# Kernel tuning notes

Measured on AMD Instinct MI355X. Metric: run time of the kernel, lower is better.

The kernel has to match this reference:

```python
import jax, jax.numpy as jnp
import numpy as np
from jax import lax

# Dims
HID = 2048          # hidden_size
DI = 4096           # d_inner = expand * hidden
NH = 64             # mamba heads
P = 64              # head dim
N = 128             # d_state
G = 1               # n_groups
K = 4               # conv kernel
IM = 8192           # MLP intermediate
BB, L = 2, 2048
EPS = 1e-5
CONV_DIM = DI + 2 * G * N            # 4352
D_IN_PROJ = 2 * DI + 2 * G * N + NH  # 8512


def rmsnorm(x, w, eps=EPS):
    v = jnp.mean(jnp.square(x), axis=-1, keepdims=True)
    return x * jax.lax.rsqrt(v + eps) * w


def setup_inputs() -> dict:
    key = jax.random.key(0)
    ks = jax.random.split(key, 16)
    s = 0.02
    return {
        "positions": jnp.broadcast_to(jnp.arange(L, dtype=jnp.int32), (BB, L)),
        "hidden_states": jax.random.normal(ks[0], (BB, L, HID), jnp.float32),
        "residual": jax.random.normal(ks[1], (BB, L, HID), jnp.float32),
        "in_proj_w": jax.random.normal(ks[2], (D_IN_PROJ, HID), jnp.float32) * s,
        "conv_w": jax.random.normal(ks[3], (CONV_DIM, K), jnp.float32) * 0.2,
        "conv_b": jax.random.normal(ks[4], (CONV_DIM,), jnp.float32) * 0.02,
        "A_log": jnp.log(jnp.arange(1, NH + 1, dtype=jnp.float32)),
        "D": jnp.ones((NH,), jnp.float32),
        "dt_bias": jax.random.uniform(ks[5], (NH,), jnp.float32, -4.0, -2.0),
        "mixer_norm_w": jnp.ones((DI,), jnp.float32),
        "out_proj_w": jax.random.normal(ks[6], (HID, DI), jnp.float32) * s,
        "input_ln_w": jnp.ones((HID,), jnp.float32),
        "pre_ff_ln_w": jnp.ones((HID,), jnp.float32),
        "gate_up_w": jax.random.normal(ks[7], (2 * IM, HID), jnp.float32) * s,
        "down_w": jax.random.normal(ks[8], (HID, IM), jnp.float32) * s,
    }


def reference(positions, hidden_states, residual, in_proj_w, conv_w, conv_b,
              A_log, D, dt_bias, mixer_norm_w, out_proj_w, input_ln_w,
              pre_ff_ln_w, gate_up_w, down_w):
    del positions  # not used by the mamba mixer math
    B_, Lq, _ = hidden_states.shape

    # --- input RMSNorm with fused residual add ---
    residual = hidden_states + residual
    hs = rmsnorm(residual, input_ln_w)

    # --- Mamba2 mixer ---
    proj = jnp.einsum('bld,ed->ble', hs, in_proj_w)   # [B,L,D_IN_PROJ]
    z = proj[..., :DI]
    xBC = proj[..., DI:DI + CONV_DIM]
    dt = proj[..., DI + CONV_DIM:]                    # [B,L,NH]

    # causal depthwise conv (kernel K) + SiLU
    xp = jnp.pad(xBC, ((0, 0), (K - 1, 0), (0, 0)))
    conv = conv_b
    for k in range(K):
        conv = conv + xp[:, k:k + Lq, :] * conv_w[:, k]
    xBC = jax.nn.silu(conv)

    x = xBC[..., :DI].reshape(B_, Lq, NH, P)
    Bm = xBC[..., DI:DI + G * N].reshape(B_, Lq, G, N)
    Cm = xBC[..., DI + G * N:].reshape(B_, Lq, G, N)
    rep = NH // G
    Bm = jnp.repeat(Bm, rep, axis=2)                  # [B,L,NH,N]
    Cm = jnp.repeat(Cm, rep, axis=2)

    dt = jax.nn.softplus(dt + dt_bias)                # [B,L,NH]
    A = -jnp.exp(A_log)                               # [NH]
    dA = jnp.exp(dt * A)                              # [B,L,NH]

    def step(h, inp):
        x_t, B_t, C_t, dA_t, dt_t = inp               # [B,NH,P],[B,NH,N],[B,NH,N],[B,NH],[B,NH]
        h = dA_t[..., None, None] * h + \
            (dt_t[..., None, None] * x_t[..., None]) * B_t[:, :, None, :]
        y = jnp.einsum('bhpn,bhn->bhp', h, C_t)
        return h, y

    xs = (x.transpose(1, 0, 2, 3), Bm.transpose(1, 0, 2, 3),
          Cm.transpose(1, 0, 2, 3), dA.transpose(1, 0, 2), dt.transpose(1, 0, 2))
    h0 = jnp.zeros((B_, NH, P, N), hidden_states.dtype)
    _, ys = lax.scan(step, h0, xs)                    # [L,B,NH,P]
    y = ys.transpose(1, 0, 2, 3) + D[None, None, :, None] * x
    y = y.reshape(B_, Lq, DI)

    # gated RMSNorm (Mixer2RMSNormGated, n_groups=1)
    y = y * jax.nn.silu(z)
    y = rmsnorm(y, mixer_norm_w)
    mamba_out = jnp.einsum('bld,hd->blh', y, out_proj_w)

    # --- pre-FF RMSNorm with fused residual add ---
    residual2 = mamba_out + residual
    hs2 = rmsnorm(residual2, pre_ff_ln_w)

    # --- gated MLP (SiluAndMul) ---
    gu = jnp.einsum('bld,ed->ble', hs2, gate_up_w)    # [B,L,2*IM]
    act = jax.nn.silu(gu[..., :IM]) * gu[..., IM:]
    out = jnp.einsum('bli,hi->blh', act, down_w)
    return out, residual2
```

## Files before the change

### kernel.cpp

```cpp
#include <hip/hip_runtime.h>

#define T_TOK 4096
#define HID   2048
#define DI    4096
#define NH    64
#define PDIM  64
#define NSTATE 128
#define IM    8192
#define LSEQ  2048
#define CONVD 4352
#define DPROJ 8512
#define DPADR 8704
#define QC    64
#define NCH   32

typedef __bf16 bf16x8 __attribute__((ext_vector_type(8)));
typedef float  f32x4  __attribute__((ext_vector_type(4)));

__device__ __forceinline__ unsigned short f2bf(float f) {
  unsigned u = __float_as_uint(f);
  u = (u + 0x7fffu + ((u >> 16) & 1u)) >> 16;
  return (unsigned short)u;
}
__device__ __forceinline__ float bf2f(unsigned short h) {
  return __uint_as_float(((unsigned)h) << 16);
}
__device__ __forceinline__ float siluf(float x) {
  return x / (1.f + __expf(-x));
}

#define GLL(gaddr, laddr) __builtin_amdgcn_global_load_lds( \
    (const __attribute__((address_space(1))) void*)(gaddr), \
    (__attribute__((address_space(3))) void*)(laddr), 16, 0, 0)

__device__ __forceinline__ void cvt8(const float* __restrict__ s, unsigned short* __restrict__ d) {
  float4 v0 = *(const float4*)s;
  float4 v1 = *(const float4*)(s + 4);
  unsigned short o[8];
  o[0] = f2bf(v0.x); o[1] = f2bf(v0.y); o[2] = f2bf(v0.z); o[3] = f2bf(v0.w);
  o[4] = f2bf(v1.x); o[5] = f2bf(v1.y); o[6] = f2bf(v1.z); o[7] = f2bf(v1.w);
  *(uint4*)d = *(const uint4*)o;
}

#define CV_IN_END  2228224ULL
#define CV_OUT_END 3276800ULL
#define CV_GU_END  7471104ULL
#define CV_DN_END  9568256ULL

__global__ __launch_bounds__(256)
void k_cvt_all(const float* __restrict__ w_in, const float* __restrict__ w_out,
               const float* __restrict__ w_gu, const float* __restrict__ w_dn,
               unsigned short* __restrict__ d_in, unsigned short* __restrict__ d_out,
               unsigned short* __restrict__ d_gu, unsigned short* __restrict__ d_dn) {
  size_t gid = (size_t)blockIdx.x * 256 + threadIdx.x;
  if (gid < CV_IN_END) {
    size_t idx8 = gid * 8;
    int r = (int)(idx8 >> 11), k = (int)(idx8 & 2047);
    if (r < DPROJ) {
      cvt8(&w_in[(size_t)r * HID + k], d_in + idx8);
    } else {
      uint4 z = {0, 0, 0, 0};
      *(uint4*)(d_in + idx8) = z;
    }
  } else if (gid < CV_OUT_END) {
    size_t idx8 = (gid - CV_IN_END) * 8;
    cvt8(w_out + idx8, d_out + idx8);
  } else if (gid < CV_GU_END) {
    size_t idx8 = (gid - CV_OUT_END) * 8;
    int r = (int)(idx8 >> 11), k = (int)(idx8 & 2047);
    int g = r >> 6, j = r & 63;
    int srcr = (j < 32) ? (g * 32 + j) : (IM + g * 32 + (j - 32));
    cvt8(&w_gu[(size_t)srcr * HID + k], d_gu + idx8);
  } else if (gid < CV_DN_END) {
    size_t idx8 = (gid - CV_GU_END) * 8;
    cvt8(w_dn + idx8, d_dn + idx8);
  }
}

template <int EPI, int BM>
__global__ __launch_bounds__(512, 2)
void gemm8(const unsigned short* __restrict__ A, const unsigned short* __restrict__ W,
           int K, int ldo, void* __restrict__ outp,
           const float* __restrict__ resid) {
  constexpr int MREP  = BM / 32;
  constexpr int ABYT  = BM * 128;
  constexpr int BUFB  = ABYT + 32768;
  constexpr int NTM   = 4096 / BM;
  __shared__ __align__(16) char smem[2 * BUFB];
  const int t = threadIdx.x;
  const int w = t >> 6, l = t & 63;
  const int lr = l & 15, hi = l >> 4;
  const int wr = w >> 2, wc = w & 3;

  const int q = (int)gridDim.x >> 3;
  const int bid = blockIdx.x;
  const int id2 = (bid & 7) * q + (bid >> 3);
  const int tn = id2 / NTM, tm = id2 % NTM;
  const int m0b = tm * BM, n0b = tn << 8;

  const int srow = t >> 3;
  const int scole = ((t & 7) << 3) ^ ((t & 32) ? 16 : 0) ^ ((t & 64) ? 32 : 0);
  const unsigned short* Ag = A + (size_t)(m0b + srow) * K + scole;
  const unsigned short* Wg = W + (size_t)(n0b + srow) * K + scole;
  const int ldsw = w * 1024;

  const int fa = ((lr & 4) ? 32 : 0) | ((lr & 8) ? 64 : 0);
  const int arow = (wr * (BM / 2) + lr) * 128 + hi * 16;
  const int brow = (wc * 64 + lr) * 128 + hi * 16;
  const int aoff0 = arow ^ fa, aoff1 = (arow + 64) ^ fa;
  const int boff0 = brow ^ fa, boff1 = (brow + 64) ^ fa;

#define ISSUE_A(jt, bb) do {                                                    \
    _Pragma("unroll")                                                           \
    for (int p_ = 0; p_ < BM / 64; ++p_)                                        \
      GLL(Ag + (size_t)(p_ * 64) * K + (size_t)(jt) * 64,                       \
          smem + (bb) * BUFB + p_ * 8192 + ldsw); } while (0)
#define ISSUE_B(jt, bb) do {                                                    \
    _Pragma("unroll")                                                           \
    for (int p_ = 0; p_ < 4; ++p_)                                              \
      GLL(Wg + (size_t)(p_ * 64) * K + (size_t)(jt) * 64,                       \
          smem + (bb) * BUFB + ABYT + p_ * 8192 + ldsw); } while (0)

#define RDF(off, base) (*(const bf16x8*)((base) + (off)))
#define MF(P, x, y, c0, c1, c2, c3) do {                                                     \
    acc[2*(P)  ][0] = __builtin_amdgcn_mfma_f32_16x16x32_bf16((x),(c0),acc[2*(P)  ][0],0,0,0);\
    acc[2*(P)+1][0] = __builtin_amdgcn_mfma_f32_16x16x32_bf16((y),(c0),acc[2*(P)+1][0],0,0,0);\
    acc[2*(P)  ][1] = __builtin_amdgcn_mfma_f32_16x16x32_bf16((x),(c1),acc[2*(P)  ][1],0,0,0);\
    acc[2*(P)+1][1] = __builtin_amdgcn_mfma_f32_16x16x32_bf16((y),(c1),acc[2*(P)+1][1],0,0,0);\
    acc[2*(P)  ][2] = __builtin_amdgcn_mfma_f32_16x16x32_bf16((x),(c2),acc[2*(P)  ][2],0,0,0);\
    acc[2*(P)+1][2] = __builtin_amdgcn_mfma_f32_16x16x32_bf16((y),(c2),acc[2*(P)+1][2],0,0,0);\
    acc[2*(P)  ][3] = __builtin_amdgcn_mfma_f32_16x16x32_bf16((x),(c3),acc[2*(P)  ][3],0,0,0);\
    acc[2*(P)+1][3] = __builtin_amdgcn_mfma_f32_16x16x32_bf16((y),(c3),acc[2*(P)+1][3],0,0,0);\
    } while (0)

  f32x4 acc[MREP][4];
#pragma unroll
  for (int m = 0; m < MREP; m++)
#pragma unroll
    for (int n = 0; n < 4; n++) acc[m][n] = (f32x4){0.f, 0.f, 0.f, 0.f};

  const int nkt = K >> 6;
  ISSUE_A(0, 0); ISSUE_B(0, 0);

  for (int j = 0; j < nkt; ++j) {
    const int cur = j & 1;
    const char* Ab = smem + cur * BUFB;
    const char* Bb = Ab + ABYT;
    asm volatile("s_waitcnt vmcnt(0)" ::: "memory");
    __builtin_amdgcn_s_barrier();
    __builtin_amdgcn_sched_barrier(0);
    if (j + 1 < nkt) { ISSUE_A(j + 1, cur ^ 1); ISSUE_B(j + 1, cur ^ 1); }
    bf16x8 b0 = RDF(boff0, Bb), b1 = RDF(boff0 + 2048, Bb),
           b2 = RDF(boff0 + 4096, Bb), b3 = RDF(boff0 + 6144, Bb);
    bf16x8 af0 = RDF(aoff0, Ab), af1 = RDF(aoff0 + 2048, Ab);
    bf16x8 af2, af3, b4, b5, b6, b7;
    if constexpr (MREP == 8) {
      af2 = RDF(aoff0 + 4096, Ab); af3 = RDF(aoff0 + 6144, Ab);
      MF(0, af0, af1, b0, b1, b2, b3);
      af0 = RDF(aoff0 + 8192, Ab); af1 = RDF(aoff0 + 10240, Ab);
      MF(1, af2, af3, b0, b1, b2, b3);
      af2 = RDF(aoff0 + 12288, Ab); af3 = RDF(aoff0 + 14336, Ab);
      MF(2, af0, af1, b0, b1, b2, b3);
      b4 = RDF(boff1, Bb); b5 = RDF(boff1 + 2048, Bb);
      b6 = RDF(boff1 + 4096, Bb); b7 = RDF(boff1 + 6144, Bb);
      af0 = RDF(aoff1, Ab); af1 = RDF(aoff1 + 2048, Ab);
      MF(3, af2, af3, b0, b1, b2, b3);
      af2 = RDF(aoff1 + 4096, Ab); af3 = RDF(aoff1 + 6144, Ab);
      MF(0, af0, af1, b4, b5, b6, b7);
      af0 = RDF(aoff1 + 8192, Ab); af1 = RDF(aoff1 + 10240, Ab);
      MF(1, af2, af3, b4, b5, b6, b7);
      af2 = RDF(aoff1 + 12288, Ab); af3 = RDF(aoff1 + 14336, Ab);
      MF(2, af0, af1, b4, b5, b6, b7);
      MF(3, af2, af3, b4, b5, b6, b7);
    } else {
      af2 = RDF(aoff0 + 4096, Ab); af3 = RDF(aoff0 + 6144, Ab);
      MF(0, af0, af1, b0, b1, b2, b3);
      b4 = RDF(boff1, Bb); b5 = RDF(boff1 + 2048, Bb);
      b6 = RDF(boff1 + 4096, Bb); b7 = RDF(boff1 + 6144, Bb);
      af0 = RDF(aoff1, Ab); af1 = RDF(aoff1 + 2048, Ab);
      MF(1, af2, af3, b0, b1, b2, b3);
      af2 = RDF(aoff1 + 4096, Ab); af3 = RDF(aoff1 + 6144, Ab);
      MF(0, af0, af1, b4, b5, b6, b7);
      MF(1, af2, af3, b4, b5, b6, b7);
    }
  }

  if constexpr (EPI == 0) {
    unsigned short* op = (unsigned short*)outp;
#pragma unroll
    for (int m = 0; m < MREP; m++)
#pragma unroll
      for (int n = 0; n < 4; n++)
#pragma unroll
        for (int r = 0; r < 4; r++) {
          int row = m0b + wr * (BM / 2) + m * 16 + hi * 4 + r;
          int col = n0b + wc * 64 + n * 16 + lr;
          op[(size_t)row * ldo + col] = f2bf(acc[m][n][r]);
        }
  } else if constexpr (EPI == 2) {
    unsigned short* op = (unsigned short*)outp;
    const int gbase = (n0b + wc * 64) >> 1;
#pragma unroll
    for (int m = 0; m < MREP; m++)
#pragma unroll
      for (int n = 0; n < 2; n++)
#pragma unroll
        for (int r = 0; r < 4; r++) {
          int row = m0b + wr * (BM / 2) + m * 16 + hi * 4 + r;
          int col = gbase + n * 16 + lr;
          float g = acc[m][n][r], u = acc[m][n + 2][r];
          op[(size_t)row * ldo + col] = f2bf(siluf(g) * u);
        }
  } else {
    float* op = (float*)outp;
#pragma unroll
    for (int m = 0; m < MREP; m++)
#pragma unroll
      for (int n = 0; n < 4; n++)
#pragma unroll
        for (int r = 0; r < 4; r++) {
          int row = m0b + wr * (BM / 2) + m * 16 + hi * 4 + r;
          int col = n0b + wc * 64 + n * 16 + lr;
          float v = acc[m][n][r];
          if constexpr (EPI == 1) v += resid[(size_t)row * ldo + col];
          op[(size_t)row * ldo + col] = v;
        }
  }
#undef ISSUE_A
#undef ISSUE_B
#undef RDF
#undef MF
}

__device__ __forceinline__ float block_reduce_sum256(float v, float* sred) {
#pragma unroll
  for (int m = 32; m; m >>= 1) v += __shfl_xor(v, m);
  int t = threadIdx.x;
  if ((t & 63) == 0) sred[t >> 6] = v;
  __syncthreads();
  return sred[0] + sred[1] + sred[2] + sred[3];
}

__global__ __launch_bounds__(256)
void k_addnorm(const float* __restrict__ hin, const float* __restrict__ rin,
               const float* __restrict__ wln, float* __restrict__ rout,
               unsigned short* __restrict__ hbf) {
  __shared__ float sred[4];
  const int tok = blockIdx.x, t = threadIdx.x;
  const size_t base = (size_t)tok * HID + t * 8;
  float4 a0 = *(const float4*)&hin[base];
  float4 a1 = *(const float4*)&hin[base + 4];
  float4 b0 = *(const float4*)&rin[base];
  float4 b1 = *(const float4*)&rin[base + 4];
  float v[8] = {a0.x + b0.x, a0.y + b0.y, a0.z + b0.z, a0.w + b0.w,
                a1.x + b1.x, a1.y + b1.y, a1.z + b1.z, a1.w + b1.w};
  float ss = 0.f;
#pragma unroll
  for (int j = 0; j < 8; j++) ss += v[j] * v[j];
  float tot = block_reduce_sum256(ss, sred);
  float rms = rsqrtf(tot * (1.f / HID) + 1e-5f);
  *(float4*)&rout[base] = (float4){v[0], v[1], v[2], v[3]};
  *(float4*)&rout[base + 4] = (float4){v[4], v[5], v[6], v[7]};
  float4 w0 = *(const float4*)&wln[t * 8];
  float4 w1 = *(const float4*)&wln[t * 8 + 4];
  float wa[8] = {w0.x, w0.y, w0.z, w0.w, w1.x, w1.y, w1.z, w1.w};
  unsigned short o[8];
#pragma unroll
  for (int j = 0; j < 8; j++) o[j] = f2bf(v[j] * rms * wa[j]);
  *(ushort4*)&hbf[base] = *(ushort4*)&o[0];
  *(ushort4*)&hbf[base + 4] = *(ushort4*)&o[4];
}

__global__ __launch_bounds__(256)
void k_rmsnorm_bf(const float* __restrict__ src, const float* __restrict__ wln,
                  unsigned short* __restrict__ dst) {
  __shared__ float sred[4];
  const int tok = blockIdx.x, t = threadIdx.x;
  const size_t base = (size_t)tok * HID + t * 8;
  float4 a0 = *(const float4*)&src[base];
  float4 a1 = *(const float4*)&src[base + 4];
  float v[8] = {a0.x, a0.y, a0.z, a0.w, a1.x, a1.y, a1.z, a1.w};
  float ss = 0.f;
#pragma unroll
  for (int j = 0; j < 8; j++) ss += v[j] * v[j];
  float tot = block_reduce_sum256(ss, sred);
  float rms = rsqrtf(tot * (1.f / HID) + 1e-5f);
  float4 w0 = *(const float4*)&wln[t * 8];
  float4 w1 = *(const float4*)&wln[t * 8 + 4];
  float wa[8] = {w0.x, w0.y, w0.z, w0.w, w1.x, w1.y, w1.z, w1.w};
  unsigned short o[8];
#pragma unroll
  for (int j = 0; j < 8; j++) o[j] = f2bf(v[j] * rms * wa[j]);
  *(ushort4*)&dst[base] = *(ushort4*)&o[0];
  *(ushort4*)&dst[base + 4] = *(ushort4*)&o[4];
}

__global__ __launch_bounds__(256)
void k_gatenorm(const unsigned short* __restrict__ ybuf, const unsigned short* __restrict__ projbf,
                const float* __restrict__ wmix, unsigned short* __restrict__ ynorm) {
  __shared__ float sred[4];
  const int tok = blockIdx.x, t = threadIdx.x;
  const size_t yb = (size_t)tok * DI;
  const size_t pb = (size_t)tok * DPADR;
  float g[16];
  float ss = 0.f;
#pragma unroll
  for (int j = 0; j < 16; j++) {
    int idx = j * 256 + t;
    float yv = bf2f(ybuf[yb + idx]);
    float z = bf2f(projbf[pb + idx]);
    float gg = yv * siluf(z);
    g[j] = gg;
    ss += gg * gg;
  }
  float tot = block_reduce_sum256(ss, sred);
  float rms = rsqrtf(tot * (1.f / DI) + 1e-5f);
#pragma unroll
  for (int j = 0; j < 16; j++) {
    int idx = j * 256 + t;
    ynorm[yb + idx] = f2bf(g[j] * rms * wmix[idx]);
  }
}

__global__ __launch_bounds__(256)
void k_conv(const unsigned short* __restrict__ projbf, const float* __restrict__ cw,
            const float* __restrict__ cb, const float* __restrict__ dt_bias,
            unsigned short* __restrict__ xbf, unsigned short* __restrict__ bcbf,
            float* __restrict__ dtg) {
  const int c = blockIdx.x * 256 + threadIdx.x;
  const int tk = blockIdx.y;
  if (c < CONVD) {
    const int lpos = tk & (LSEQ - 1);
    float4 wv = *(const float4*)&cw[c * 4];
    float wk[4] = {wv.x, wv.y, wv.z, wv.w};
    float acc = cb[c];
#pragma unroll
    for (int k = 0; k < 4; k++) {
      int lp = lpos - 3 + k;
      if (lp >= 0) acc += bf2f(projbf[(size_t)(tk - 3 + k) * DPADR + DI + c]) * wk[k];
    }
    unsigned short r = f2bf(siluf(acc));
    if (c < DI) xbf[(size_t)tk * DI + c] = r;
    else        bcbf[(size_t)tk * 256 + (c - DI)] = r;
  } else if (c < CONVD + NH) {
    const int hh = c - CONVD;
    float x = bf2f(projbf[(size_t)tk * DPADR + DI + c]) + dt_bias[hh];
    float dt = (x > 20.f) ? x : log1pf(__expf(x));
    dtg[(size_t)tk * NH + hh] = dt;
  }
}

__global__ __launch_bounds__(256)
void k_ssd1(const unsigned short* __restrict__ xbf, const unsigned short* __restrict__ bcbf,
            const float* __restrict__ dtg, const float* __restrict__ A_log,
            const float* __restrict__ Dv, unsigned short* __restrict__ ybuf,
            unsigned short* __restrict__ Sc, float* __restrict__ dtsum) {
  __shared__ __align__(16) char smem[60928];
  unsigned short* sBs  = (unsigned short*)(smem);
  unsigned short* sCs  = (unsigned short*)(smem + 16384);
  unsigned short* sMs  = (unsigned short*)(smem + 16384);
  unsigned short* sBsT = (unsigned short*)(smem + 32768);
  unsigned short* sXsT = (unsigned short*)(smem + 51200);
  float* sdt = (float*)(smem + 60416);
  float* sdl = (float*)(smem + 60672);

  const int bi = blockIdx.x;
  const int ch = bi & 31, h = (bi >> 5) & 63, b = bi >> 11;
  const int bh = b * NH + h;
  const int tok0 = b * LSEQ + ch * QC;
  const int t = threadIdx.x;
  const int w = t >> 6, l = t & 63, lr = l & 15, hi = l >> 4;
  const float Ah = -__expf(A_log[h]);
  const float Dh = Dv[h];

  {
    const int srow = t >> 4, scol = (t & 15) * 8;
#pragma unroll
    for (int i = 0; i < 4; i++) {
      const unsigned short* gb = bcbf + (size_t)(tok0 + srow + 16 * i) * 256 + scol;
      GLL(gb, (char*)sBs + i * 4096 + w * 1024);
      GLL(gb + 128, (char*)sCs + i * 4096 + w * 1024);
    }
  }
  if (t < QC) sdt[t] = dtg[(size_t)(tok0 + t) * NH + h];
  __syncthreads();
  if (t < QC) sdl[t] = sdt[t];
  __syncthreads();
  for (int off = 1; off < QC; off <<= 1) {
    float v = 0.f;
    if (t < QC && t >= off) v = sdl[t - off];
    __syncthreads();
    if (t < QC) sdl[t] += v;
    __syncthreads();
  }

  {
    const int s = t >> 2;
    const float DlQ = sdl[QC - 1];
    const float csc = __expf(Ah * (DlQ - sdl[s])) * sdt[s];
    const int n0 = (t & 3) * 32;
#pragma unroll
    for (int j = 0; j < 32; j++) {
      float bv = bf2f(sBs[s * 128 + n0 + j]);
      sBsT[(n0 + j) * 72 + s] = f2bf(csc * bv);
    }
    const int p0 = (t & 3) * 16;
    const unsigned short* gx = xbf + (size_t)(tok0 + s) * DI + h * 64 + p0;
    union { uint4 v; unsigned short u[8]; } x0, x1;
    x0.v = *(const uint4*)gx;
    x1.v = *(const uint4*)(gx + 8);
#pragma unroll
    for (int j = 0; j < 8; j++) {
      sXsT[(p0 + j) * 72 + s] = x0.u[j];
      sXsT[(p0 + 8 + j) * 72 + s] = x1.u[j];
    }
  }
  __syncthreads();

  f32x4 accS[4];
#pragma unroll
  for (int jf = 0; jf < 4; jf++) accS[jf] = (f32x4){0.f, 0.f, 0.f, 0.f};
#pragma unroll
  for (int ks = 0; ks < 4; ks++) {
    bf16x8 a = *(const bf16x8*)&sBs[(w * 16 + lr) * 128 + ks * 32 + hi * 8];
#pragma unroll
    for (int jf = 0; jf < 4; jf++) {
      bf16x8 bbq = *(const bf16x8*)&sCs[(jf * 16 + lr) * 128 + ks * 32 + hi * 8];
      accS[jf] = __builtin_amdgcn_mfma_f32_16x16x32_bf16(a, bbq, accS[jf], 0, 0, 0);
    }
  }
  __syncthreads();

  {
    const int s0 = w * 16 + hi * 4;
#pragma unroll
    for (int jf = 0; jf < 4; jf++) {
      const int tt = jf * 16 + lr;
      const float dlt = sdl[tt];
      unsigned short mv[4];
#pragma unroll
      for (int r = 0; r < 4; r++) {
        const int ss = s0 + r;
        float val = 0.f;
        if (ss <= tt) val = accS[jf][r] * __expf(Ah * (dlt - sdl[ss])) * sdt[ss];
        mv[r] = f2bf(val);
      }
      *(ushort4*)&sMs[tt * 72 + s0] = *(ushort4*)mv;
    }
  }
  __syncthreads();

  {
    f32x4 accY[4];
#pragma unroll
    for (int jf = 0; jf < 4; jf++) accY[jf] = (f32x4){0.f, 0.f, 0.f, 0.f};
#pragma unroll
    for (int ks = 0; ks < 2; ks++) {
      bf16x8 a = *(const bf16x8*)&sMs[(w * 16 + lr) * 72 + ks * 32 + hi * 8];
#pragma unroll
      for (int jf = 0; jf < 4; jf++) {
        bf16x8 bbq = *(const bf16x8*)&sXsT[(jf * 16 + lr) * 72 + ks * 32 + hi * 8];
        accY[jf] = __builtin_amdgcn_mfma_f32_16x16x32_bf16(a, bbq, accY[jf], 0, 0, 0);
      }
    }
#pragma unroll
    for (int jf = 0; jf < 4; jf++)
#pragma unroll
      for (int r = 0; r < 4; r++) {
        const int tt = w * 16 + hi * 4 + r;
        const int pp = jf * 16 + lr;
        float xv = bf2f(sXsT[pp * 72 + tt]);
        ybuf[(size_t)(tok0 + tt) * DI + h * 64 + pp] = f2bf(accY[jf][r] + Dh * xv);
      }
  }

  {
    f32x4 accT[8];
#pragma unroll
    for (int jf = 0; jf < 8; jf++) accT[jf] = (f32x4){0.f, 0.f, 0.f, 0.f};
#pragma unroll
    for (int ks = 0; ks < 2; ks++) {
      bf16x8 a = *(const bf16x8*)&sXsT[(w * 16 + lr) * 72 + ks * 32 + hi * 8];
#pragma unroll
      for (int jf = 0; jf < 8; jf++) {
        bf16x8 bbq = *(const bf16x8*)&sBsT[(jf * 16 + lr) * 72 + ks * 32 + hi * 8];
        accT[jf] = __builtin_amdgcn_mfma_f32_16x16x32_bf16(a, bbq, accT[jf], 0, 0, 0);
      }
    }
    unsigned short* sc = Sc + ((size_t)bh * NCH + ch) * (PDIM * NSTATE);
#pragma unroll
    for (int jf = 0; jf < 8; jf++)
#pragma unroll
      for (int r = 0; r < 4; r++) {
        const int pp = w * 16 + hi * 4 + r;
        const int nn = jf * 16 + lr;
        sc[pp * NSTATE + nn] = f2bf(accT[jf][r]);
      }
  }
  if (t == 0) dtsum[bh * NCH + ch] = sdl[QC - 1];
}

__global__ __launch_bounds__(256)
void k_ssd2(const float* __restrict__ A_log, const float* __restrict__ dtsum,
            unsigned short* __restrict__ ScHt) {
  const int blk = blockIdx.x;
  const int bh = blk >> 3, pg = blk & 7;
  const int t = threadIdx.x;
  const int p = pg * 8 + (t >> 5), n0 = (t & 31) * 4;
  const int h = bh & 63;
  const float Ah = -__expf(A_log[h]);
  float H[4] = {0.f, 0.f, 0.f, 0.f};
  for (int c = 0; c < NCH; c++) {
    size_t base = (((size_t)bh * NCH + c) * PDIM + p) * NSTATE + n0;
    ushort4 sv = *(const ushort4*)&ScHt[base];
    float dec = __expf(Ah * dtsum[bh * NCH + c]);
    ushort4 hv;
    hv.x = f2bf(H[0]); hv.y = f2bf(H[1]); hv.z = f2bf(H[2]); hv.w = f2bf(H[3]);
    *(ushort4*)&ScHt[base] = hv;
    H[0] = dec * H[0] + bf2f(sv.x);
    H[1] = dec * H[1] + bf2f(sv.y);
    H[2] = dec * H[2] + bf2f(sv.z);
    H[3] = dec * H[3] + bf2f(sv.w);
  }
}

__global__ __launch_bounds__(256)
void k_ssd3(const unsigned short* __restrict__ bcbf, const unsigned short* __restrict__ Ht,
            const float* __restrict__ dtg, const float* __restrict__ A_log,
            unsigned short* __restrict__ ybuf) {
  __shared__ __align__(16) char smem[33280];
  unsigned short* sCs = (unsigned short*)(smem);
  unsigned short* sHt = (unsigned short*)(smem + 16384);
  float* sdt = (float*)(smem + 32768);
  float* sdl = (float*)(smem + 33024);

  const int bi = blockIdx.x;
  const int ch = bi & 31, h = (bi >> 5) & 63, b = bi >> 11;
  const int bh = b * NH + h;
  const int tok0 = b * LSEQ + ch * QC;
  const int t = threadIdx.x;
  const int w = t >> 6, l = t & 63, lr = l & 15, hi = l >> 4;
  const float Ah = -__expf(A_log[h]);

  {
    const int srow = t >> 4, scol = (t & 15) * 8;
    const unsigned short* gh = Ht + ((size_t)bh * NCH + ch) * (PDIM * NSTATE);
#pragma unroll
    for (int i = 0; i < 4; i++) {
      const unsigned short* gc = bcbf + (size_t)(tok0 + srow + 16 * i) * 256 + 128 + scol;
      GLL(gc, (char*)sCs + i * 4096 + w * 1024);
      GLL(gh + i * 2048 + t * 8, (char*)sHt + i * 4096 + w * 1024);
    }
  }
  if (t < QC) sdt[t] = dtg[(size_t)(tok0 + t) * NH + h];
  __syncthreads();
  if (t < QC) sdl[t] = sdt[t];
  __syncthreads();
  for (int off = 1; off < QC; off <<= 1) {
    float v = 0.f;
    if (t < QC && t >= off) v = sdl[t - off];
    __syncthreads();
    if (t < QC) sdl[t] += v;
    __syncthreads();
  }

  f32x4 acc[4];
#pragma unroll
  for (int jf = 0; jf < 4; jf++) acc[jf] = (f32x4){0.f, 0.f, 0.f, 0.f};
#pragma unroll
  for (int ks = 0; ks < 4; ks++) {
    bf16x8 a = *(const bf16x8*)&sCs[(w * 16 + lr) * 128 + ks * 32 + hi * 8];
#pragma unroll
    for (int jf = 0; jf < 4; jf++) {
      bf16x8 bbq = *(const bf16x8*)&sHt[(jf * 16 + lr) * 128 + ks * 32 + hi * 8];
      acc[jf] = __builtin_amdgcn_mfma_f32_16x16x32_bf16(a, bbq, acc[jf], 0, 0, 0);
    }
  }
#pragma unroll
  for (int jf = 0; jf < 4; jf++)
#pragma unroll
    for (int r = 0; r < 4; r++) {
      const int tt = w * 16 + hi * 4 + r;
      const int pp = jf * 16 + lr;
      const float dec = __expf(Ah * sdl[tt]);
      const size_t o = (size_t)(tok0 + tt) * DI + h * 64 + pp;
      ybuf[o] = f2bf(bf2f(ybuf[o]) + dec * acc[jf][r]);
    }
}

static const size_t OFF_WBF_IN  = 0;
static const size_t OFF_WBF_OUT = 35651584;
static const size_t OFF_WBF_GU  = 52428800;
static const size_t OFF_WBF_DN  = 119537664;
static const size_t OFF_RESID   = 153092096;
static const size_t OFF_HSBF    = 186646528;
static const size_t OFF_PROJ    = 203423744;
static const size_t OFF_XBF     = 274726912;
static const size_t OFF_BCBF    = 308281344;
static const size_t OFF_DTG     = 310378496;
static const size_t OFF_YBUF    = 311427072;
static const size_t OFF_SC      = 344981504;
static const size_t OFF_DTSUM   = 412090368;

extern "C" void kernel_launch(void* const* d_in, const int* in_sizes, int n_in,
                              void* d_out, int out_size, void* d_ws, size_t ws_size,
                              hipStream_t stream) {
  (void)in_sizes; (void)n_in; (void)out_size; (void)ws_size;
  const float* hidden   = (const float*)d_in[1];
  const float* resin    = (const float*)d_in[2];
  const float* w_inproj = (const float*)d_in[3];
  const float* conv_w   = (const float*)d_in[4];
  const float* conv_b   = (const float*)d_in[5];
  const float* A_log    = (const float*)d_in[6];
  const float* Dvec     = (const float*)d_in[7];
  const float* dt_bias  = (const float*)d_in[8];
  const float* w_mix    = (const float*)d_in[9];
  const float* w_outp   = (const float*)d_in[10];
  const float* w_ln1    = (const float*)d_in[11];
  const float* w_ln2    = (const float*)d_in[12];
  const float* w_gu     = (const float*)d_in[13];
  const float* w_dn     = (const float*)d_in[14];

  char* ws = (char*)d_ws;
  unsigned short* wbf_in  = (unsigned short*)(ws + OFF_WBF_IN);
  unsigned short* wbf_out = (unsigned short*)(ws + OFF_WBF_OUT);
  unsigned short* wbf_gu  = (unsigned short*)(ws + OFF_WBF_GU);
  unsigned short* wbf_dn  = (unsigned short*)(ws + OFF_WBF_DN);
  float*          residb  = (float*)(ws + OFF_RESID);
  unsigned short* hsbf    = (unsigned short*)(ws + OFF_HSBF);
  unsigned short* projbf  = (unsigned short*)(ws + OFF_PROJ);
  unsigned short* actbf   = (unsigned short*)(ws + OFF_PROJ);
  unsigned short* xbf     = (unsigned short*)(ws + OFF_XBF);
  unsigned short* ynormbf = (unsigned short*)(ws + OFF_XBF);
  unsigned short* bcbf    = (unsigned short*)(ws + OFF_BCBF);
  float*          dtgb    = (float*)(ws + OFF_DTG);
  unsigned short* ybuf    = (unsigned short*)(ws + OFF_YBUF);
  unsigned short* scht    = (unsigned short*)(ws + OFF_SC);
  float*          dtsumb  = (float*)(ws + OFF_DTSUM);

  float* out0 = (float*)d_out;
  float* res2 = out0 + (size_t)T_TOK * HID;

  k_cvt_all<<<37376, 256, 0, stream>>>(w_inproj, w_outp, w_gu, w_dn,
                                       wbf_in, wbf_out, wbf_gu, wbf_dn);
  k_addnorm<<<T_TOK, 256, 0, stream>>>(hidden, resin, w_ln1, residb, hsbf);
  gemm8<0, 256><<<34 * 16, 512, 0, stream>>>(hsbf, wbf_in, HID, DPADR, projbf, nullptr);
  k_conv<<<dim3(18, T_TOK), 256, 0, stream>>>(projbf, conv_w, conv_b, dt_bias, xbf, bcbf, dtgb);
  k_ssd1<<<4096, 256, 0, stream>>>(xbf, bcbf, dtgb, A_log, Dvec, ybuf, scht, dtsumb);
  k_ssd2<<<1024, 256, 0, stream>>>(A_log, dtsumb, scht);
  k_ssd3<<<4096, 256, 0, stream>>>(bcbf, scht, dtgb, A_log, ybuf);
  k_gatenorm<<<T_TOK, 256, 0, stream>>>(ybuf, projbf, w_mix, ynormbf);
  gemm8<1, 128><<<8 * 32, 512, 0, stream>>>(ynormbf, wbf_out, DI, HID, res2, residb);
  k_rmsnorm_bf<<<T_TOK, 256, 0, stream>>>(res2, w_ln2, hsbf);
  gemm8<2, 256><<<64 * 16, 512, 0, stream>>>(hsbf, wbf_gu, HID, IM, actbf, nullptr);
  gemm8<3, 128><<<8 * 32, 512, 0, stream>>>(actbf, wbf_dn, IM, HID, out0, nullptr);
}
```

Baseline: 994.8 us.

## Fuse weight conversion into addnorm and in_proj GEMM launches for overlap

Removes the standalone weight-conversion kernel. The in_proj weight conversion is appended as extra blocks to the addnorm kernel, and the out_proj, gate_up and down weight conversions are appended as extra blocks to the in_proj GEMM kernel. This lets the memory-bound conversion overlap with the addnorm and GEMM work and removes one launch. In exchange, the conversion blocks inherit the GEMM kernel's shared memory and launch bounds, and they compete with the GEMM for bandwidth.

```diff
diff --git a/kernel.cpp b/kernel.cpp
--- a/kernel.cpp
+++ b/kernel.cpp
@@ -47,12 +47,11 @@
 #define CV_GU_END  7471104ULL
 #define CV_DN_END  9568256ULL
 
-__global__ __launch_bounds__(256)
-void k_cvt_all(const float* __restrict__ w_in, const float* __restrict__ w_out,
-               const float* __restrict__ w_gu, const float* __restrict__ w_dn,
-               unsigned short* __restrict__ d_in, unsigned short* __restrict__ d_out,
-               unsigned short* __restrict__ d_gu, unsigned short* __restrict__ d_dn) {
-  size_t gid = (size_t)blockIdx.x * 256 + threadIdx.x;
+__device__ __forceinline__ void cvt_do(size_t gid,
+    const float* __restrict__ w_in, const float* __restrict__ w_out,
+    const float* __restrict__ w_gu, const float* __restrict__ w_dn,
+    unsigned short* __restrict__ d_in, unsigned short* __restrict__ d_out,
+    unsigned short* __restrict__ d_gu, unsigned short* __restrict__ d_dn) {
   if (gid < CV_IN_END) {
     size_t idx8 = gid * 8;
     int r = (int)(idx8 >> 11), k = (int)(idx8 & 2047);
@@ -78,10 +77,9 @@
 }
 
 template <int EPI, int BM>
-__global__ __launch_bounds__(512, 2)
-void gemm8(const unsigned short* __restrict__ A, const unsigned short* __restrict__ W,
-           int K, int ldo, void* __restrict__ outp,
-           const float* __restrict__ resid) {
+__device__ __forceinline__ void gemm_body(int bid, int ngb,
+    const unsigned short* __restrict__ A, const unsigned short* __restrict__ W,
+    int K, int ldo, void* __restrict__ outp, const float* __restrict__ resid) {
   constexpr int MREP  = BM / 32;
   constexpr int ABYT  = BM * 128;
   constexpr int BUFB  = ABYT + 32768;
@@ -92,8 +90,7 @@
   const int lr = l & 15, hi = l >> 4;
   const int wr = w >> 2, wc = w & 3;
 
-  const int q = (int)gridDim.x >> 3;
-  const int bid = blockIdx.x;
+  const int q = ngb >> 3;
   const int id2 = (bid & 7) * q + (bid >> 3);
   const int tn = id2 / NTM, tm = id2 % NTM;
   const int m0b = tm * BM, n0b = tn << 8;
@@ -232,6 +229,27 @@
 #undef MF
 }
 
+template <int EPI, int BM>
+__global__ __launch_bounds__(512, 2)
+void gemm8(const unsigned short* __restrict__ A, const unsigned short* __restrict__ W,
+           int K, int ldo, void* __restrict__ outp, const float* __restrict__ resid) {
+  gemm_body<EPI, BM>((int)blockIdx.x, (int)gridDim.x, A, W, K, ldo, outp, resid);
+}
+
+__global__ __launch_bounds__(512, 2)
+void k_inproj_fused(const unsigned short* __restrict__ A, const unsigned short* __restrict__ Wbf,
+                    int ngb, unsigned short* __restrict__ projbf,
+                    const float* __restrict__ w_out, const float* __restrict__ w_gu,
+                    const float* __restrict__ w_dn, unsigned short* __restrict__ d_out,
+                    unsigned short* __restrict__ d_gu, unsigned short* __restrict__ d_dn) {
+  if ((int)blockIdx.x < ngb) {
+    gemm_body<0, 256>((int)blockIdx.x, ngb, A, Wbf, HID, DPADR, projbf, nullptr);
+  } else {
+    size_t gid = CV_IN_END + (size_t)((int)blockIdx.x - ngb) * 512 + threadIdx.x;
+    cvt_do(gid, nullptr, w_out, w_gu, w_dn, nullptr, d_out, d_gu, d_dn);
+  }
+}
+
 __device__ __forceinline__ float block_reduce_sum256(float v, float* sred) {
 #pragma unroll
   for (int m = 32; m; m >>= 1) v += __shfl_xor(v, m);
@@ -244,7 +262,13 @@
 __global__ __launch_bounds__(256)
 void k_addnorm(const float* __restrict__ hin, const float* __restrict__ rin,
                const float* __restrict__ wln, float* __restrict__ rout,
-               unsigned short* __restrict__ hbf) {
+               unsigned short* __restrict__ hbf,
+               const float* __restrict__ w_in, unsigned short* __restrict__ d_in) {
+  if ((int)blockIdx.x >= T_TOK) {
+    size_t gid = (size_t)((int)blockIdx.x - T_TOK) * 256 + threadIdx.x;
+    cvt_do(gid, w_in, nullptr, nullptr, nullptr, d_in, nullptr, nullptr, nullptr);
+    return;
+  }
   __shared__ float sred[4];
   const int tok = blockIdx.x, t = threadIdx.x;
   const size_t base = (size_t)tok * HID + t * 8;
@@ -641,10 +665,11 @@
   float* out0 = (float*)d_out;
   float* res2 = out0 + (size_t)T_TOK * HID;
 
-  k_cvt_all<<<37376, 256, 0, stream>>>(w_inproj, w_outp, w_gu, w_dn,
-                                       wbf_in, wbf_out, wbf_gu, wbf_dn);
-  k_addnorm<<<T_TOK, 256, 0, stream>>>(hidden, resin, w_ln1, residb, hsbf);
-  gemm8<0, 256><<<34 * 16, 512, 0, stream>>>(hsbf, wbf_in, HID, DPADR, projbf, nullptr);
+  k_addnorm<<<T_TOK + 8704, 256, 0, stream>>>(hidden, resin, w_ln1, residb, hsbf,
+                                              w_inproj, wbf_in);
+  k_inproj_fused<<<544 + 14336, 512, 0, stream>>>(hsbf, wbf_in, 544, projbf,
+                                                  w_outp, w_gu, w_dn,
+                                                  wbf_out, wbf_gu, wbf_dn);
   k_conv<<<dim3(18, T_TOK), 256, 0, stream>>>(projbf, conv_w, conv_b, dt_bias, xbf, bcbf, dtgb);
   k_ssd1<<<4096, 256, 0, stream>>>(xbf, bcbf, dtgb, A_log, Dvec, ybuf, scht, dtsumb);
   k_ssd2<<<1024, 256, 0, stream>>>(A_log, dtsumb, scht);
```

Result: no change. 987.0 us, median of 3 (-0.8%).
